# Performance work log

Measured on AMD Instinct MI355X. Metric: run time of the kernel, lower is better.

Reference implementation:

```python
import jax, jax.numpy as jnp
import numpy as np
from jax.scipy.special import logsumexp

B, T = 32, 512
WV, CV = 32000, 8000
DW, DC = 128, 64
H = 128          # hidden per direction (hidden_size // 2)
L = 32           # num_labels


def setup_inputs() -> dict:
    key = jax.random.key(0)
    ks = jax.random.split(key, 16)
    D = DW + DC
    def n(k, shape, s=0.1):
        return jax.random.normal(k, shape, jnp.float32) * s
    return {
        'word': jax.random.randint(ks[0], (B, T), 1, WV),
        'char': jax.random.randint(ks[1], (B, T), 1, CV),  # >0 so mask is all ones
        'y': jax.random.randint(ks[2], (B, T), 0, L),
        'wordemb': n(ks[3], (WV, DW)),
        'charemb': n(ks[4], (CV, DC)),
        'W_ih_f': n(ks[5], (4 * H, D)), 'W_hh_f': n(ks[6], (4 * H, H)), 'b_f': n(ks[7], (4 * H,)),
        'W_ih_b': n(ks[8], (4 * H, D)), 'W_hh_b': n(ks[9], (4 * H, H)), 'b_b': n(ks[10], (4 * H,)),
        'W_out': n(ks[11], (L, 2 * H)), 'b_out': n(ks[12], (L,)),
        'trans': n(ks[13], (L, L)), 'start': n(ks[14], (L,)), 'end': n(ks[15], (L,)),
    }


def _lstm_scan(x_proj, W_hh):
    # x_proj: [T, B, 4H] = x @ W_ih.T + b, precomputed (batched GEMM)
    h0 = jnp.zeros((x_proj.shape[1], W_hh.shape[1]), x_proj.dtype)
    def step(carry, xt):
        h, c = carry
        g = xt + h @ W_hh.T                      # [B, 4H]
        i, f, gg, o = jnp.split(g, 4, axis=-1)   # PyTorch gate order i,f,g,o
        c = jax.nn.sigmoid(f) * c + jax.nn.sigmoid(i) * jnp.tanh(gg)
        h = jax.nn.sigmoid(o) * jnp.tanh(c)
        return (h, c), h
    _, hs = jax.lax.scan(step, (h0, h0), x_proj)
    return hs  # [T, B, H]


def reference(word, char, y, wordemb, charemb, W_ih_f, W_hh_f, b_f,
              W_ih_b, W_hh_b, b_b, W_out, b_out, trans, start, end):
    mask = (char > 0).astype(jnp.float32)                 # [B, T]
    x = jnp.concatenate([wordemb[word], charemb[char]], axis=-1)  # [B, T, D]

    # BiLSTM
    xp_f = (jnp.einsum('btd,gd->tbg', x, W_ih_f) + b_f)   # [T, B, 4H]
    xp_b = (jnp.einsum('btd,gd->tbg', x, W_ih_b) + b_b)[::-1]
    h_f = _lstm_scan(xp_f, W_hh_f)                        # [T, B, H]
    h_b = _lstm_scan(xp_b, W_hh_b)[::-1]                  # [T, B, H]
    h = jnp.concatenate([h_f, h_b], axis=-1).transpose(1, 0, 2)  # [B, T, 2H]

    emit = (jnp.einsum('bth,lh->btl', h, W_out) + b_out) * mask[:, :, None]  # [B, T, L]

    # CRF log-partition (forward algorithm)
    alpha0 = start + emit[:, 0]                           # [B, L]
    def crf_step(alpha, inp):
        e_t, m_t = inp                                    # [B, L], [B]
        new = logsumexp(alpha[:, :, None] + trans, axis=1) + e_t
        alpha = jnp.where(m_t[:, None] > 0, new, alpha)
        return alpha, None
    alpha, _ = jax.lax.scan(crf_step, alpha0,
                            (emit.transpose(1, 0, 2)[1:], mask.T[1:]))
    logZ = logsumexp(alpha + end, axis=-1)                # [B]

    # gold path score
    emit_score = (jnp.take_along_axis(emit, y[:, :, None], axis=-1)[..., 0] * mask).sum(1)
    trans_score = (trans[y[:, :-1], y[:, 1:]] * mask[:, 1:]).sum(1)
    last = mask.sum(1).astype(jnp.int32) - 1
    y_last = y[jnp.arange(y.shape[0]), last]
    gold = start[y[:, 0]] + emit_score + trans_score + end[y_last]

    return jnp.sum(logZ - gold)  # NLL, summed over batch
```

## Files before the change

kernel.cpp:

```cpp
#include <hip/hip_runtime.h>
#include <math.h>

#define BB 32
#define TT 512
#define DW 128
#define DC 64
#define DD 192
#define HH 128
#define G4 512
#define LL 32

typedef __fp16 h2_t __attribute__((ext_vector_type(2)));

__device__ __forceinline__ float qxor1(float x) {
    return __int_as_float(__builtin_amdgcn_update_dpp(0, __float_as_int(x), 0xB1, 0xF, 0xF, true));
}
__device__ __forceinline__ float qxor2(float x) {
    return __int_as_float(__builtin_amdgcn_update_dpp(0, __float_as_int(x), 0x4E, 0xF, 0xF, true));
}
__device__ __forceinline__ float qbcast(float x, int ctrl_imm) {
    switch (ctrl_imm) {
        case 0: return __int_as_float(__builtin_amdgcn_update_dpp(0, __float_as_int(x), 0x00, 0xF, 0xF, true));
        case 1: return __int_as_float(__builtin_amdgcn_update_dpp(0, __float_as_int(x), 0x55, 0xF, 0xF, true));
        case 2: return __int_as_float(__builtin_amdgcn_update_dpp(0, __float_as_int(x), 0xAA, 0xF, 0xF, true));
        default:return __int_as_float(__builtin_amdgcn_update_dpp(0, __float_as_int(x), 0xFF, 0xF, 0xF, true));
    }
}

__global__ __launch_bounds__(256) void k_inproj(
    const int* __restrict__ word, const int* __restrict__ charr,
    const float* __restrict__ wemb, const float* __restrict__ cemb,
    const float* __restrict__ Wf, const float* __restrict__ bf,
    const float* __restrict__ Wb, const float* __restrict__ bb,
    float* __restrict__ xpf, float* __restrict__ xpb)
{
    __shared__ __align__(16) h2_t As2[4][132];
    __shared__ __align__(16) h2_t Bs2[4][132];
    const int tid = threadIdx.x;
    const int ntile = blockIdx.x;
    const int ctile = blockIdx.y;
    const int dir = ctile >> 2;
    const float* W = dir ? Wb : Wf;
    const float* bias = dir ? bb : bf;
    float* xp = dir ? xpb : xpf;
    const int colbase = (ctile & 3) * 128;

    const int tr = tid >> 4;
    const int tc = tid & 15;

    float acc[8][8];
#pragma unroll
    for (int i = 0; i < 8; ++i)
#pragma unroll
        for (int j = 0; j < 8; ++j) acc[i][j] = 0.f;

    const int lrow = tid >> 1;
    const int lk   = (tid & 1) * 4;
    const int kp0  = lk >> 1;
    const int nA   = ntile * 128 + lrow;
    const int wi   = word[nA];
    const int ci   = charr[nA];
    const int g    = colbase + lrow;

    for (int kc = 0; kc < 24; ++kc) {
        const int k0 = kc * 8 + lk;
        float4 av;
        if (k0 < DW) av = *(const float4*)(wemb + (size_t)wi * DW + k0);
        else         av = *(const float4*)(cemb + (size_t)ci * DC + (k0 - DW));
        const float4 bv = *(const float4*)(W + (size_t)g * DD + k0);
        __syncthreads();
        As2[kp0 + 0][lrow] = __builtin_amdgcn_cvt_pkrtz(av.x, av.y);
        As2[kp0 + 1][lrow] = __builtin_amdgcn_cvt_pkrtz(av.z, av.w);
        Bs2[kp0 + 0][lrow] = __builtin_amdgcn_cvt_pkrtz(bv.x, bv.y);
        Bs2[kp0 + 1][lrow] = __builtin_amdgcn_cvt_pkrtz(bv.z, bv.w);
        __syncthreads();
#pragma unroll
        for (int kp = 0; kp < 4; ++kp) {
            h2_t __attribute__((aligned(16))) a2[8], b2[8];
            *(uint4*)&a2[0] = *(const uint4*)&As2[kp][tr * 8];
            *(uint4*)&a2[4] = *(const uint4*)&As2[kp][tr * 8 + 4];
            *(uint4*)&b2[0] = *(const uint4*)&Bs2[kp][tc * 8];
            *(uint4*)&b2[4] = *(const uint4*)&Bs2[kp][tc * 8 + 4];
#pragma unroll
            for (int i = 0; i < 8; ++i)
#pragma unroll
                for (int j = 0; j < 8; ++j)
                    acc[i][j] = __builtin_amdgcn_fdot2(a2[i], b2[j], acc[i][j], false);
        }
    }
#pragma unroll
    for (int i = 0; i < 8; ++i) {
        const int n  = ntile * 128 + tr * 8 + i;
        const int b_ = n >> 9, t_ = n & 511;
        float* dst = xp + ((size_t)(t_ * BB + b_)) * G4 + colbase + tc * 8;
#pragma unroll
        for (int j = 0; j < 8; ++j) dst[j] = acc[i][j] + bias[colbase + tc * 8 + j];
    }
}

__global__ __launch_bounds__(512)
__attribute__((amdgpu_waves_per_eu(2, 2)))
void k_lstm(
    const float* __restrict__ xpf, const float* __restrict__ xpb,
    const float* __restrict__ Whf, const float* __restrict__ Whb,
    float* __restrict__ hf, float* __restrict__ hb)
{
    __shared__ __align__(16) __fp16 hsd[2][160];
    const int tid = threadIdx.x;
    const int dir = blockIdx.x >> 5;
    const int b_  = blockIdx.x & 31;
    const float* xp = dir ? xpb : xpf;
    const float* Wh = dir ? Whb : Whf;
    float* hout = dir ? hb : hf;
    const int ks = tid & 3;
    const int u  = tid >> 2;

    h2_t w2[4][16];
#pragma unroll
    for (int g = 0; g < 4; ++g) {
        const float2* wp = (const float2*)(Wh + (size_t)(g * 128 + u) * HH + ks * 32);
#pragma unroll
        for (int j = 0; j < 16; ++j)
            w2[g][j] = __builtin_amdgcn_cvt_pkrtz(wp[j].x, wp[j].y);
    }

    const float mk0 = (ks == 0) ? 1.f : 0.f;
    const float mk1 = (ks == 1) ? 1.f : 0.f;
    const float mk2 = (ks == 2) ? 1.f : 0.f;
    const float mk3 = (ks == 3) ? 1.f : 0.f;
    const bool istanh = (ks == 2);
    const float GS  = istanh ? 2.f : -1.f;
    const float GC0 = istanh ? 1.f : 0.f;
    const float GC1 = istanh ? -2.f : 1.f;
    const bool ks1 = (ks & 1) != 0;
    const bool ks2 = (ks & 2) != 0;

    if (tid < 80) ((unsigned int*)&hsd[0][0])[tid] = 0u;
    float c = 0.f;
    const int t0 = dir ? (TT - 1) : 0;
    const int tstep = dir ? -1 : 1;
    const int xstride = tstep * BB * G4;
    const int hstride = tstep * BB * HH;
    const float* xqp = xp + ((long long)t0 * BB + b_) * G4 + ks * 128 + u;
    float*       hop = hout + ((long long)t0 * BB + b_) * HH + u;
    float xq = *xqp;
    __syncthreads();

    for (int s = 0; s < TT; ++s) {
        const int rb = s & 1;
        float p0 = mk0 * xq, p1 = mk1 * xq, p2 = mk2 * xq, p3 = mk3 * xq;
        xqp += xstride;
        xq = *xqp;
#pragma unroll
        for (int q = 0; q < 4; ++q) {
            const uint4 hv = *(const uint4*)&hsd[rb][ks * 40 + q * 8];
            const h2_t ha  = __builtin_bit_cast(h2_t, hv.x);
            const h2_t hbv = __builtin_bit_cast(h2_t, hv.y);
            const h2_t hc  = __builtin_bit_cast(h2_t, hv.z);
            const h2_t hd  = __builtin_bit_cast(h2_t, hv.w);
            p0 = __builtin_amdgcn_fdot2(ha,  w2[0][q*4+0], p0, false);
            p0 = __builtin_amdgcn_fdot2(hbv, w2[0][q*4+1], p0, false);
            p0 = __builtin_amdgcn_fdot2(hc,  w2[0][q*4+2], p0, false);
            p0 = __builtin_amdgcn_fdot2(hd,  w2[0][q*4+3], p0, false);
            p1 = __builtin_amdgcn_fdot2(ha,  w2[1][q*4+0], p1, false);
            p1 = __builtin_amdgcn_fdot2(hbv, w2[1][q*4+1], p1, false);
            p1 = __builtin_amdgcn_fdot2(hc,  w2[1][q*4+2], p1, false);
            p1 = __builtin_amdgcn_fdot2(hd,  w2[1][q*4+3], p1, false);
            p2 = __builtin_amdgcn_fdot2(ha,  w2[2][q*4+0], p2, false);
            p2 = __builtin_amdgcn_fdot2(hbv, w2[2][q*4+1], p2, false);
            p2 = __builtin_amdgcn_fdot2(hc,  w2[2][q*4+2], p2, false);
            p2 = __builtin_amdgcn_fdot2(hd,  w2[2][q*4+3], p2, false);
            p3 = __builtin_amdgcn_fdot2(ha,  w2[3][q*4+0], p3, false);
            p3 = __builtin_amdgcn_fdot2(hbv, w2[3][q*4+1], p3, false);
            p3 = __builtin_amdgcn_fdot2(hc,  w2[3][q*4+2], p3, false);
            p3 = __builtin_amdgcn_fdot2(hd,  w2[3][q*4+3], p3, false);
        }
        p0 += qxor1(p0); p0 += qxor2(p0);
        p1 += qxor1(p1); p1 += qxor2(p1);
        p2 += qxor1(p2); p2 += qxor2(p2);
        p3 += qxor1(p3); p3 += qxor2(p3);
        const float pa   = ks1 ? p1 : p0;
        const float pb   = ks1 ? p3 : p2;
        const float psel = ks2 ? pb : pa;
        const float val  = GC0 + GC1 * __builtin_amdgcn_rcpf(1.f + __expf(GS * psel));
        const float gi = qbcast(val, 0);
        const float gf = qbcast(val, 1);
        const float gg = qbcast(val, 2);
        const float go = qbcast(val, 3);
        c = gf * c + gi * gg;
        const float tc = 1.f - 2.f * __builtin_amdgcn_rcpf(1.f + __expf(2.f * c));
        const float hv = go * tc;
        if (ks == 0) {
            hsd[rb ^ 1][(u >> 5) * 40 + (u & 31)] = (__fp16)hv;
            *hop = hv;
        }
        hop += hstride;
        __builtin_amdgcn_sched_barrier(0);
        asm volatile("s_waitcnt lgkmcnt(0)");
        __builtin_amdgcn_s_barrier();
        __builtin_amdgcn_sched_barrier(0);
    }
}

__global__ __launch_bounds__(1024) void k_emit(
    const float* __restrict__ hf, const float* __restrict__ hb,
    const float* __restrict__ Wout, const float* __restrict__ bout,
    const int* __restrict__ charr, float* __restrict__ emit)
{
    __shared__ __align__(16) float hsm[BB * 256];
    __shared__ __align__(16) float wsm[LL * 260];
    const int t = blockIdx.x;
    const int tid = threadIdx.x;
    for (int idx = tid; idx < BB * 256; idx += 1024) {
        const int b_ = idx >> 8, u = idx & 255;
        hsm[idx] = (u < HH) ? hf[((size_t)t * BB + b_) * HH + u]
                            : hb[((size_t)t * BB + b_) * HH + (u - HH)];
    }
    for (int idx = tid; idx < LL * 256; idx += 1024) {
        const int l = idx >> 8, u = idx & 255;
        wsm[l * 260 + u] = Wout[idx];
    }
    __syncthreads();
    const int b_ = tid >> 5, l = tid & 31;
    float acc = bout[l];
#pragma unroll 8
    for (int q = 0; q < 64; ++q) {
        const float4 h4 = *(const float4*)&hsm[b_ * 256 + q * 4];
        const float4 w4 = *(const float4*)&wsm[l * 260 + q * 4];
        acc += h4.x * w4.x + h4.y * w4.y + h4.z * w4.z + h4.w * w4.w;
    }
    const float m = (charr[b_ * TT + t] > 0) ? 1.f : 0.f;
    emit[((size_t)t * BB + b_) * LL + l] = acc * m;
}

__global__ __launch_bounds__(64) void k_crf(
    const float* __restrict__ emit, const int* __restrict__ charr,
    const float* __restrict__ trans, const float* __restrict__ startv,
    const float* __restrict__ endv, float* __restrict__ logZ)
{
    const int tid = threadIdx.x;
    const int b_ = blockIdx.x;
    const int j = tid & 31;
    float et[32];
#pragma unroll
    for (int i = 0; i < 32; ++i) et[i] = __expf(trans[i * LL + j]);

    const float a0 = startv[j] + emit[(size_t)b_ * LL + j];
    float M = a0;
    M = fmaxf(M, __shfl_xor(M, 16));
    M = fmaxf(M, __shfl_xor(M, 8));
    M = fmaxf(M, __shfl_xor(M, 4));
    M = fmaxf(M, __shfl_xor(M, 2));
    M = fmaxf(M, __shfl_xor(M, 1));
    float A = __expf(a0 - M);
    float logsc = M;

    float e_nx = emit[((size_t)1 * BB + b_) * LL + j];
    int   m_nx = charr[b_ * TT + 1];

    for (int t = 1; t < TT; ++t) {
        const float ee = __expf(e_nx);
        const int m_cur = m_nx;
        if (t + 1 < TT) {
            e_nx = emit[((size_t)(t + 1) * BB + b_) * LL + j];
            m_nx = charr[b_ * TT + t + 1];
        }
        float s0 = 0.f, s1 = 0.f, s2 = 0.f, s3 = 0.f;
#pragma unroll
        for (int i = 0; i < 32; i += 4) {
            s0 = fmaf(__shfl(A, i    ), et[i    ], s0);
            s1 = fmaf(__shfl(A, i + 1), et[i + 1], s1);
            s2 = fmaf(__shfl(A, i + 2), et[i + 2], s2);
            s3 = fmaf(__shfl(A, i + 3), et[i + 3], s3);
        }
        const float Anew = ((s0 + s1) + (s2 + s3)) * ee;
        A = (m_cur > 0) ? Anew : A;
        if ((t & 7) == 0) {
            float S = A;
            S = fmaxf(S, __shfl_xor(S, 16));
            S = fmaxf(S, __shfl_xor(S, 8));
            S = fmaxf(S, __shfl_xor(S, 4));
            S = fmaxf(S, __shfl_xor(S, 2));
            S = fmaxf(S, __shfl_xor(S, 1));
            A *= __builtin_amdgcn_rcpf(S);
            logsc += __logf(S);
        }
    }
    const float z = __logf(A) + logsc + endv[j];
    float Mz = z;
    Mz = fmaxf(Mz, __shfl_xor(Mz, 16));
    Mz = fmaxf(Mz, __shfl_xor(Mz, 8));
    Mz = fmaxf(Mz, __shfl_xor(Mz, 4));
    Mz = fmaxf(Mz, __shfl_xor(Mz, 2));
    Mz = fmaxf(Mz, __shfl_xor(Mz, 1));
    float sz = __expf(z - Mz);
    sz += __shfl_xor(sz, 16);
    sz += __shfl_xor(sz, 8);
    sz += __shfl_xor(sz, 4);
    sz += __shfl_xor(sz, 2);
    sz += __shfl_xor(sz, 1);
    if (tid == 0) logZ[b_] = Mz + __logf(sz);
}

__global__ __launch_bounds__(1024) void k_gold(
    const float* __restrict__ emit, const int* __restrict__ charr,
    const int* __restrict__ y, const float* __restrict__ trans,
    const float* __restrict__ startv, const float* __restrict__ endv,
    const float* __restrict__ logZ, float* __restrict__ out)
{
    __shared__ float red[BB];
    const int tid = threadIdx.x;
    const int b_ = tid >> 5, l = tid & 31;
    float sc = 0.f;
    int ms = 0;
    for (int t = l; t < TT; t += 32) {
        const int yv = y[b_ * TT + t];
        const int m = (charr[b_ * TT + t] > 0);
        if (m) { sc += emit[((size_t)t * BB + b_) * LL + yv]; ms++; }
        if (t + 1 < TT) {
            const int mn = (charr[b_ * TT + t + 1] > 0);
            if (mn) sc += trans[yv * LL + y[b_ * TT + t + 1]];
        }
    }
#pragma unroll
    for (int o = 16; o; o >>= 1) {
        sc += __shfl_xor(sc, o);
        ms += __shfl_xor(ms, o);
    }
    if (l == 0) {
        int last = ms - 1;
        if (last < 0) last = 0;
        const float gold = startv[y[b_ * TT]] + sc + endv[y[b_ * TT + last]];
        red[b_] = logZ[b_] - gold;
    }
    __syncthreads();
    if (tid == 0) {
        float tot = 0.f;
#pragma unroll
        for (int i = 0; i < BB; ++i) tot += red[i];
        out[0] = tot;
    }
}

extern "C" void kernel_launch(void* const* d_in, const int* in_sizes, int n_in,
                              void* d_out, int out_size, void* d_ws, size_t ws_size,
                              hipStream_t stream) {
    (void)in_sizes; (void)n_in; (void)out_size; (void)ws_size;
    const int*   word  = (const int*)d_in[0];
    const int*   charr = (const int*)d_in[1];
    const int*   yv    = (const int*)d_in[2];
    const float* wemb  = (const float*)d_in[3];
    const float* cemb  = (const float*)d_in[4];
    const float* Wihf  = (const float*)d_in[5];
    const float* Whhf  = (const float*)d_in[6];
    const float* bf    = (const float*)d_in[7];
    const float* Wihb  = (const float*)d_in[8];
    const float* Whhb  = (const float*)d_in[9];
    const float* bb    = (const float*)d_in[10];
    const float* Wout  = (const float*)d_in[11];
    const float* bout  = (const float*)d_in[12];
    const float* trans = (const float*)d_in[13];
    const float* startv= (const float*)d_in[14];
    const float* endv  = (const float*)d_in[15];

    float* ws   = (float*)d_ws;
    float* xpf  = ws;
    float* xpb  = xpf + (size_t)TT * BB * G4;
    float* hf   = xpb + (size_t)TT * BB * G4;
    float* hb   = hf + (size_t)TT * BB * HH;
    float* emit = hb + (size_t)TT * BB * HH;
    float* logZ = emit + (size_t)TT * BB * LL;

    k_inproj<<<dim3(128, 8), 256, 0, stream>>>(word, charr, wemb, cemb,
                                               Wihf, bf, Wihb, bb, xpf, xpb);
    k_lstm<<<64, 512, 0, stream>>>(xpf, xpb, Whhf, Whhb, hf, hb);
    k_emit<<<TT, 1024, 0, stream>>>(hf, hb, Wout, bout, charr, emit);
    k_crf<<<32, 64, 0, stream>>>(emit, charr, trans, startv, endv, logZ);
    k_gold<<<1, 1024, 0, stream>>>(emit, charr, yv, trans, startv, endv, logZ,
                                   (float*)d_out);
}
```

Measured before the change: 537.1 us.

## Restructure LSTM gate mapping, use rational tanh, prefetch inproj loads, readlane in CRF

The LSTM kernel now gives each thread one full gate row (a 128-long dot product) instead of splitting four gates across four lanes. This removes the DPP cross-lane reductions and the select logic, at the cost of more LDS broadcast reads of h. Sigmoid and tanh are replaced by a clamped Padé rational approximation, which avoids exp but adds some approximation error. The input-projection GEMM prefetches the next K-chunk's global loads before the compute loop. The CRF recursion uses readlane instead of shfl, taking the broadcasts off the LDS path.

After: 521.9 us. -2.8%, faster.

```diff
diff --git a/kernel.cpp b/kernel.cpp
--- a/kernel.cpp
+++ b/kernel.cpp
@@ -12,12 +12,8 @@
 
 typedef __fp16 h2_t __attribute__((ext_vector_type(2)));
 
-__device__ __forceinline__ float qxor1(float x) {
-    return __int_as_float(__builtin_amdgcn_update_dpp(0, __float_as_int(x), 0xB1, 0xF, 0xF, true));
-}
-__device__ __forceinline__ float qxor2(float x) {
-    return __int_as_float(__builtin_amdgcn_update_dpp(0, __float_as_int(x), 0x4E, 0xF, 0xF, true));
-}
+__device__ __forceinline__ h2_t bch2(unsigned int x) { return __builtin_bit_cast(h2_t, x); }
+
 __device__ __forceinline__ float qbcast(float x, int ctrl_imm) {
     switch (ctrl_imm) {
         case 0: return __int_as_float(__builtin_amdgcn_update_dpp(0, __float_as_int(x), 0x00, 0xF, 0xF, true));
@@ -25,6 +21,18 @@
         case 2: return __int_as_float(__builtin_amdgcn_update_dpp(0, __float_as_int(x), 0xAA, 0xF, 0xF, true));
         default:return __int_as_float(__builtin_amdgcn_update_dpp(0, __float_as_int(x), 0xFF, 0xF, 0xF, true));
     }
+}
+
+__device__ __forceinline__ float rtanh(float x) {
+    x = fminf(fmaxf(x, -8.f), 8.f);
+    const float x2 = x * x;
+    const float pa = 378.f + x2;
+    const float pb = fmaf(x2, pa, 17325.f);
+    const float pc = fmaf(x2, pb, 135135.f);
+    const float qa = fmaf(x2, 28.f, 3150.f);
+    const float qb = fmaf(x2, qa, 62370.f);
+    const float qq = fmaf(x2, qb, 135135.f);
+    return x * pc * __builtin_amdgcn_rcpf(qq);
 }
 
 __global__ __launch_bounds__(256) void k_inproj(
@@ -62,18 +70,22 @@
     const int ci   = charr[nA];
     const int g    = colbase + lrow;
 
+    float4 av = *(const float4*)(wemb + (size_t)wi * DW + lk);
+    float4 bv = *(const float4*)(W + (size_t)g * DD + lk);
+
     for (int kc = 0; kc < 24; ++kc) {
-        const int k0 = kc * 8 + lk;
-        float4 av;
-        if (k0 < DW) av = *(const float4*)(wemb + (size_t)wi * DW + k0);
-        else         av = *(const float4*)(cemb + (size_t)ci * DC + (k0 - DW));
-        const float4 bv = *(const float4*)(W + (size_t)g * DD + k0);
         __syncthreads();
         As2[kp0 + 0][lrow] = __builtin_amdgcn_cvt_pkrtz(av.x, av.y);
         As2[kp0 + 1][lrow] = __builtin_amdgcn_cvt_pkrtz(av.z, av.w);
         Bs2[kp0 + 0][lrow] = __builtin_amdgcn_cvt_pkrtz(bv.x, bv.y);
         Bs2[kp0 + 1][lrow] = __builtin_amdgcn_cvt_pkrtz(bv.z, bv.w);
         __syncthreads();
+        const int kcn = (kc + 1 < 24) ? (kc + 1) : 23;
+        const int k0n = kcn * 8 + lk;
+        float4 avn, bvn;
+        if (k0n < DW) avn = *(const float4*)(wemb + (size_t)wi * DW + k0n);
+        else          avn = *(const float4*)(cemb + (size_t)ci * DC + (k0n - DW));
+        bvn = *(const float4*)(W + (size_t)g * DD + k0n);
 #pragma unroll
         for (int kp = 0; kp < 4; ++kp) {
             h2_t __attribute__((aligned(16))) a2[8], b2[8];
@@ -87,6 +99,7 @@
                 for (int j = 0; j < 8; ++j)
                     acc[i][j] = __builtin_amdgcn_fdot2(a2[i], b2[j], acc[i][j], false);
         }
+        av = avn; bv = bvn;
     }
 #pragma unroll
     for (int i = 0; i < 8; ++i) {
@@ -105,7 +118,7 @@
     const float* __restrict__ Whf, const float* __restrict__ Whb,
     float* __restrict__ hf, float* __restrict__ hb)
 {
-    __shared__ __align__(16) __fp16 hsd[2][160];
+    __shared__ __align__(16) __fp16 hsd[2][HH];
     const int tid = threadIdx.x;
     const int dir = blockIdx.x >> 5;
     const int b_  = blockIdx.x & 31;
@@ -115,27 +128,20 @@
     const int ks = tid & 3;
     const int u  = tid >> 2;
 
-    h2_t w2[4][16];
-#pragma unroll
-    for (int g = 0; g < 4; ++g) {
-        const float2* wp = (const float2*)(Wh + (size_t)(g * 128 + u) * HH + ks * 32);
-#pragma unroll
-        for (int j = 0; j < 16; ++j)
-            w2[g][j] = __builtin_amdgcn_cvt_pkrtz(wp[j].x, wp[j].y);
-    }
-
-    const float mk0 = (ks == 0) ? 1.f : 0.f;
-    const float mk1 = (ks == 1) ? 1.f : 0.f;
-    const float mk2 = (ks == 2) ? 1.f : 0.f;
-    const float mk3 = (ks == 3) ? 1.f : 0.f;
+    h2_t w2[64];
+    {
+        const float2* wp = (const float2*)(Wh + (size_t)(ks * 128 + u) * HH);
+#pragma unroll
+        for (int j = 0; j < 64; ++j)
+            w2[j] = __builtin_amdgcn_cvt_pkrtz(wp[j].x, wp[j].y);
+    }
+
     const bool istanh = (ks == 2);
-    const float GS  = istanh ? 2.f : -1.f;
-    const float GC0 = istanh ? 1.f : 0.f;
-    const float GC1 = istanh ? -2.f : 1.f;
-    const bool ks1 = (ks & 1) != 0;
-    const bool ks2 = (ks & 2) != 0;
-
-    if (tid < 80) ((unsigned int*)&hsd[0][0])[tid] = 0u;
+    const float SC = istanh ? 1.f : 0.5f;
+    const float C0 = istanh ? 0.f : 0.5f;
+    const float C1 = istanh ? 1.f : 0.5f;
+
+    if (tid < 64) ((unsigned int*)&hsd[0][0])[tid] = 0u;
     float c = 0.f;
     const int t0 = dir ? (TT - 1) : 0;
     const int tstep = dir ? -1 : 1;
@@ -148,51 +154,27 @@
 
     for (int s = 0; s < TT; ++s) {
         const int rb = s & 1;
-        float p0 = mk0 * xq, p1 = mk1 * xq, p2 = mk2 * xq, p3 = mk3 * xq;
+        float p = xq;
         xqp += xstride;
         xq = *xqp;
 #pragma unroll
-        for (int q = 0; q < 4; ++q) {
-            const uint4 hv = *(const uint4*)&hsd[rb][ks * 40 + q * 8];
-            const h2_t ha  = __builtin_bit_cast(h2_t, hv.x);
-            const h2_t hbv = __builtin_bit_cast(h2_t, hv.y);
-            const h2_t hc  = __builtin_bit_cast(h2_t, hv.z);
-            const h2_t hd  = __builtin_bit_cast(h2_t, hv.w);
-            p0 = __builtin_amdgcn_fdot2(ha,  w2[0][q*4+0], p0, false);
-            p0 = __builtin_amdgcn_fdot2(hbv, w2[0][q*4+1], p0, false);
-            p0 = __builtin_amdgcn_fdot2(hc,  w2[0][q*4+2], p0, false);
-            p0 = __builtin_amdgcn_fdot2(hd,  w2[0][q*4+3], p0, false);
-            p1 = __builtin_amdgcn_fdot2(ha,  w2[1][q*4+0], p1, false);
-            p1 = __builtin_amdgcn_fdot2(hbv, w2[1][q*4+1], p1, false);
-            p1 = __builtin_amdgcn_fdot2(hc,  w2[1][q*4+2], p1, false);
-            p1 = __builtin_amdgcn_fdot2(hd,  w2[1][q*4+3], p1, false);
-            p2 = __builtin_amdgcn_fdot2(ha,  w2[2][q*4+0], p2, false);
-            p2 = __builtin_amdgcn_fdot2(hbv, w2[2][q*4+1], p2, false);
-            p2 = __builtin_amdgcn_fdot2(hc,  w2[2][q*4+2], p2, false);
-            p2 = __builtin_amdgcn_fdot2(hd,  w2[2][q*4+3], p2, false);
-            p3 = __builtin_amdgcn_fdot2(ha,  w2[3][q*4+0], p3, false);
-            p3 = __builtin_amdgcn_fdot2(hbv, w2[3][q*4+1], p3, false);
-            p3 = __builtin_amdgcn_fdot2(hc,  w2[3][q*4+2], p3, false);
-            p3 = __builtin_amdgcn_fdot2(hd,  w2[3][q*4+3], p3, false);
-        }
-        p0 += qxor1(p0); p0 += qxor2(p0);
-        p1 += qxor1(p1); p1 += qxor2(p1);
-        p2 += qxor1(p2); p2 += qxor2(p2);
-        p3 += qxor1(p3); p3 += qxor2(p3);
-        const float pa   = ks1 ? p1 : p0;
-        const float pb   = ks1 ? p3 : p2;
-        const float psel = ks2 ? pb : pa;
-        const float val  = GC0 + GC1 * __builtin_amdgcn_rcpf(1.f + __expf(GS * psel));
+        for (int q = 0; q < 16; ++q) {
+            const uint4 hv = *(const uint4*)&hsd[rb][q * 8];
+            p = __builtin_amdgcn_fdot2(bch2(hv.x), w2[q * 4 + 0], p, false);
+            p = __builtin_amdgcn_fdot2(bch2(hv.y), w2[q * 4 + 1], p, false);
+            p = __builtin_amdgcn_fdot2(bch2(hv.z), w2[q * 4 + 2], p, false);
+            p = __builtin_amdgcn_fdot2(bch2(hv.w), w2[q * 4 + 3], p, false);
+        }
+        const float val = fmaf(rtanh(SC * p), C1, C0);
         const float gi = qbcast(val, 0);
         const float gf = qbcast(val, 1);
         const float gg = qbcast(val, 2);
         const float go = qbcast(val, 3);
         c = gf * c + gi * gg;
-        const float tc = 1.f - 2.f * __builtin_amdgcn_rcpf(1.f + __expf(2.f * c));
-        const float hv = go * tc;
+        const float hv_ = go * rtanh(c);
         if (ks == 0) {
-            hsd[rb ^ 1][(u >> 5) * 40 + (u & 31)] = (__fp16)hv;
-            *hop = hv;
+            hsd[rb ^ 1][u] = (__fp16)hv_;
+            *hop = hv_;
         }
         hop += hstride;
         __builtin_amdgcn_sched_barrier(0);
@@ -268,10 +250,10 @@
         float s0 = 0.f, s1 = 0.f, s2 = 0.f, s3 = 0.f;
 #pragma unroll
         for (int i = 0; i < 32; i += 4) {
-            s0 = fmaf(__shfl(A, i    ), et[i    ], s0);
-            s1 = fmaf(__shfl(A, i + 1), et[i + 1], s1);
-            s2 = fmaf(__shfl(A, i + 2), et[i + 2], s2);
-            s3 = fmaf(__shfl(A, i + 3), et[i + 3], s3);
+            s0 = fmaf(__int_as_float(__builtin_amdgcn_readlane(__float_as_int(A), i    )), et[i    ], s0);
+            s1 = fmaf(__int_as_float(__builtin_amdgcn_readlane(__float_as_int(A), i + 1)), et[i + 1], s1);
+            s2 = fmaf(__int_as_float(__builtin_amdgcn_readlane(__float_as_int(A), i + 2)), et[i + 2], s2);
+            s3 = fmaf(__int_as_float(__builtin_amdgcn_readlane(__float_as_int(A), i + 3)), et[i + 3], s3);
         }
         const float Anew = ((s0 + s1) + (s2 + s3)) * ee;
         A = (m_cur > 0) ? Anew : A;
```
